# Performance work log

Measured on AMD Instinct MI355X. Metric: run time of the kernel, lower is better.

The kernel has to match this reference:

```python
import jax, jax.numpy as jnp
import numpy as np

L, B, E = 128, 16, 512
C_OUT = 64
KERNELS = [1, 3, 5, 7]
M = len(KERNELS) * C_OUT          # mlpdec_in = 256
OUT_SIZE = 256
SLOPE = 0.1


def setup_inputs() -> dict:
    key = jax.random.key(0)
    ks = jax.random.split(key, 32)
    s = 0.02
    d = {"x": jax.random.normal(ks[0], (L, B, E), dtype=jnp.float32)}
    # conv branches: weight (C_out, 1, k, E), bias (C_out,)
    for i, k in enumerate(KERNELS):
        d[f"cw{i}"] = jax.random.normal(ks[1 + 2 * i], (C_OUT, 1, k, E), dtype=jnp.float32) * s
        d[f"cb{i}"] = jnp.zeros((C_OUT,), dtype=jnp.float32)
    dims = [(C_OUT, 2 * M), (C_OUT, C_OUT), (C_OUT, C_OUT), (C_OUT, C_OUT)]
    for i, (o, inn) in enumerate(dims):
        d[f"mw{i}"] = jax.random.normal(ks[10 + 2 * i], (o, inn), dtype=jnp.float32) * s
        d[f"mb{i}"] = jnp.zeros((o,), dtype=jnp.float32)
    # mlp_layer: Linear(C->C), Linear(C->output_size)
    d["lw0"] = jax.random.normal(ks[20], (C_OUT, C_OUT), dtype=jnp.float32) * s
    d["lb0"] = jnp.zeros((C_OUT,), dtype=jnp.float32)
    d["lw1"] = jax.random.normal(ks[21], (OUT_SIZE, C_OUT), dtype=jnp.float32) * s
    d["lb1"] = jnp.zeros((OUT_SIZE,), dtype=jnp.float32)
    return d


def _lrelu(x):
    return jax.nn.leaky_relu(x, SLOPE)


def _conv_branch(xb, w, b):
    # xb: (B,1,L,E), w: (C,1,k,E) -> (B,C,L)
    k = w.shape[2]
    pad = (k - 1) // 2
    y = jax.lax.conv_general_dilated(
        xb, w, window_strides=(1, 1), padding=[(pad, pad), (0, 0)],
        dimension_numbers=("NCHW", "OIHW", "NCHW"))
    return _lrelu(y[..., 0] + b[None, :, None])


def reference(x, cw0, cb0, cw1, cb1, cw2, cb2, cw3, cb3,
              mw0, mb0, mw1, mb1, mw2, mb2, mw3, mb3,
              lw0, lb0, lw1, lb1):
    # x: (L,B,E) -> (B,1,L,E)
    xb = jnp.transpose(x, (1, 0, 2))[:, None, :, :]
    feats = jnp.concatenate([
        _conv_branch(xb, cw0, cb0), _conv_branch(xb, cw1, cb1),
        _conv_branch(xb, cw2, cb2), _conv_branch(xb, cw3, cb3)], axis=1)  # (B, 4C, L)
    f = jnp.transpose(feats, (2, 0, 1))  # (L, B, M)
    # pairwise: pair[i, j] = [f[j], f[i]]  -> (L, L, B, 2M)
    a = jnp.broadcast_to(f[None, :, :, :], (L, L, B, M))
    bpart = jnp.broadcast_to(f[:, None, :, :], (L, L, B, M))
    h = jnp.concatenate([a, bpart], axis=-1)
    for w, bb in ((mw0, mb0), (mw1, mb1), (mw2, mb2), (mw3, mb3)):
        h = _lrelu(h @ w.T + bb)
    h = h.sum(axis=0)  # (L, B, C)
    h = _lrelu(h @ lw0.T + lb0)
    return _lrelu(h @ lw1.T + lb1)  # (L, B, OUT_SIZE)
```

## Files before the change

### kernel.cpp

```cpp
#include <hip/hip_runtime.h>
#include <hip/hip_bf16.h>

#define SLOPE 0.1f
typedef unsigned short u16;
typedef unsigned int u32;
typedef __attribute__((ext_vector_type(8))) short short8;
typedef __attribute__((ext_vector_type(4))) float floatx4;

__device__ __forceinline__ float lrelu(float x) { return x > 0.0f ? x : SLOPE * x; }

__device__ __forceinline__ void split_rn(float x, u16* h, u16* l) {
    union { __hip_bfloat16 b; u16 u; } c1, c2;
    c1.b = __float2bfloat16(x);
    float hf = __bfloat162float(c1.b);
    c2.b = __float2bfloat16(x - hf);
    *h = c1.u; *l = c2.u;
}

__device__ __forceinline__ void pack2x2(float v0, float v1, u32& h, u32& l) {
    u32 a0 = __float_as_uint(v0), a1 = __float_as_uint(v1);
    h = __builtin_amdgcn_perm(a1, a0, 0x07060302u);
    float r0 = v0 - __uint_as_float(a0 & 0xFFFF0000u);
    float r1 = v1 - __uint_as_float(a1 & 0xFFFF0000u);
    l = __builtin_amdgcn_perm(__float_as_uint(r1), __float_as_uint(r0), 0x07060302u);
}

__device__ __forceinline__ short8 load_frag(const u16* p) {
    union { uint4 q; short8 s; } cv;
    cv.q = *(const uint4*)p;
    return cv.s;
}

__device__ __forceinline__ floatx4 mfma16(short8 a, short8 b, floatx4 c) {
    return __builtin_amdgcn_mfma_f32_16x16x32_bf16(a, b, c, 0, 0, 0);
}

__global__ __launch_bounds__(256) void p0_prep(
    const float* __restrict__ x,
    const float* __restrict__ cw0, const float* __restrict__ cw1,
    const float* __restrict__ cw2, const float* __restrict__ cw3,
    const float* __restrict__ mw0, const float* __restrict__ mw1,
    const float* __restrict__ mw2, const float* __restrict__ mw3,
    const float* __restrict__ lw0, const float* __restrict__ lw1,
    u16* __restrict__ xfh, u16* __restrict__ xfl,
    u16* __restrict__ wcfh, u16* __restrict__ wcfl,
    u16* __restrict__ b2fh, u16* __restrict__ b2fl,
    u16* __restrict__ w3fh, u16* __restrict__ w3fl,
    float* __restrict__ lw0t, float* __restrict__ lw1t)
{
    int idx = (blockIdx.x * 256 + threadIdx.x) * 4;
    if (idx < 1048576) {
        const int j = idx & 7, lane = (idx >> 3) & 63;
        const int kc = (idx >> 9) & 15, rt = idx >> 13;
        const int l15 = lane & 15, quad = lane >> 4;
        const float4 s = *(const float4*)(x + (rt * 16 + l15) * 512 + kc * 32 + quad * 8 + j);
        u16 h[4], l[4];
        split_rn(s.x, &h[0], &l[0]); split_rn(s.y, &h[1], &l[1]);
        split_rn(s.z, &h[2], &l[2]); split_rn(s.w, &h[3], &l[3]);
        *(ushort4*)(xfh + idx) = make_ushort4(h[0], h[1], h[2], h[3]);
        *(ushort4*)(xfl + idx) = make_ushort4(l[0], l[1], l[2], l[3]);
        return;
    }
    idx -= 1048576;
    if (idx < 524288) {
        const int j = idx & 7, lane = (idx >> 3) & 63;
        const int kc = (idx >> 9) & 15, nt = (idx >> 13) & 3, slot = idx >> 15;
        int branch, base;
        if (slot == 0)      { branch = 0; base = 0; }
        else if (slot < 4)  { branch = 1; base = 1; }
        else if (slot < 9)  { branch = 2; base = 4; }
        else                { branch = 3; base = 9; }
        const int dk = slot - base, ksz = 2 * branch + 1;
        const float* cw = branch == 0 ? cw0 : branch == 1 ? cw1 : branch == 2 ? cw2 : cw3;
        const int c = nt * 16 + (lane & 15);
        const int e = kc * 32 + (lane >> 4) * 8 + j;
        const float4 s = *(const float4*)(cw + (c * ksz + dk) * 512 + e);
        u16 h[4], l[4];
        split_rn(s.x, &h[0], &l[0]); split_rn(s.y, &h[1], &l[1]);
        split_rn(s.z, &h[2], &l[2]); split_rn(s.w, &h[3], &l[3]);
        *(ushort4*)(wcfh + idx) = make_ushort4(h[0], h[1], h[2], h[3]);
        *(ushort4*)(wcfl + idx) = make_ushort4(l[0], l[1], l[2], l[3]);
        return;
    }
    idx -= 524288;
    if (idx < 32768) {
        const int j = idx & 7, lane = (idx >> 3) & 63;
        const int kc = (idx >> 9) & 7, nt = (idx >> 12) & 3, nh = idx >> 14;
        const int n = nh * 64 + nt * 16 + (lane & 15);
        const int k = kc * 32 + (lane >> 4) * 8 + j;
        const float4 s = *(const float4*)(mw0 + (n & 63) * 512 + (n >> 6) * 256 + k);
        u16 h[4], l[4];
        split_rn(s.x, &h[0], &l[0]); split_rn(s.y, &h[1], &l[1]);
        split_rn(s.z, &h[2], &l[2]); split_rn(s.w, &h[3], &l[3]);
        *(ushort4*)(b2fh + idx) = make_ushort4(h[0], h[1], h[2], h[3]);
        *(ushort4*)(b2fl + idx) = make_ushort4(l[0], l[1], l[2], l[3]);
        return;
    }
    idx -= 32768;
    if (idx < 12288) {
        const int j = idx & 7, lane = (idx >> 3) & 63;
        const int kc = (idx >> 9) & 1, mt = (idx >> 10) & 3, layer = idx >> 12;
        const float* mw = layer == 0 ? mw1 : layer == 1 ? mw2 : mw3;
        const int ch = mt * 16 + (lane & 15);
        const int k = kc * 32 + (lane >> 4) * 8 + j;
        const float4 s = *(const float4*)(mw + ch * 64 + k);
        u16 h[4], l[4];
        split_rn(s.x, &h[0], &l[0]); split_rn(s.y, &h[1], &l[1]);
        split_rn(s.z, &h[2], &l[2]); split_rn(s.w, &h[3], &l[3]);
        *(ushort4*)(w3fh + idx) = make_ushort4(h[0], h[1], h[2], h[3]);
        *(ushort4*)(w3fl + idx) = make_ushort4(l[0], l[1], l[2], l[3]);
        return;
    }
    idx -= 12288;
    if (idx < 4096) {
        const int k = idx >> 6, n = idx & 63;
        float4 o;
        o.x = lw0[(n + 0) * 64 + k]; o.y = lw0[(n + 1) * 64 + k];
        o.z = lw0[(n + 2) * 64 + k]; o.w = lw0[(n + 3) * 64 + k];
        *(float4*)(lw0t + idx) = o;
        return;
    }
    idx -= 4096;
    if (idx < 16384) {
        const int k = idx >> 8, n = idx & 255;
        float4 o;
        o.x = lw1[(n + 0) * 64 + k]; o.y = lw1[(n + 1) * 64 + k];
        o.z = lw1[(n + 2) * 64 + k]; o.w = lw1[(n + 3) * 64 + k];
        *(float4*)(lw1t + idx) = o;
        return;
    }
}

__global__ __launch_bounds__(512) void k1f_conv(
    const u16* __restrict__ xfh, const u16* __restrict__ xfl,
    const u16* __restrict__ wcfh, const u16* __restrict__ wcfl,
    float* __restrict__ Fp)
{
    __shared__ float P[8][16][72];

    const int t = threadIdx.x, lane = t & 63, w = t >> 6;
    const int rtp = blockIdx.x;
    const int slot = blockIdx.y;
    int br, base;
    if (slot == 0)      { br = 0; base = 0; }
    else if (slot < 4)  { br = 1; base = 1; }
    else if (slot < 9)  { br = 2; base = 4; }
    else                { br = 3; base = 9; }
    const int dk = slot - base;
    const int l15 = lane & 15, quad = lane >> 4;

    floatx4 acc[2][4];
    #pragma unroll
    for (int r = 0; r < 2; ++r)
        #pragma unroll
        for (int j = 0; j < 4; ++j) acc[r][j] = (floatx4)0.0f;

    #pragma unroll
    for (int kk = 0; kk < 2; ++kk) {
        const int kc = w * 2 + kk;
        short8 bh[4], bl[4];
        #pragma unroll
        for (int nt = 0; nt < 4; ++nt) {
            const int boff = (((slot * 4 + nt) * 16 + kc) * 64 + lane) * 8;
            bh[nt] = load_frag(wcfh + boff);
            bl[nt] = load_frag(wcfl + boff);
        }
        #pragma unroll
        for (int r = 0; r < 2; ++r) {
            const int rts = rtp + r * 64 + dk - br;
            if (rts < 0 || rts >= 128) continue;
            const int aoff = ((rts * 16 + kc) * 64 + lane) * 8;
            const short8 ah = load_frag(xfh + aoff);
            const short8 al = load_frag(xfl + aoff);
            #pragma unroll
            for (int nt = 0; nt < 4; ++nt) {
                acc[r][nt] = mfma16(ah, bh[nt], acc[r][nt]);
                acc[r][nt] = mfma16(ah, bl[nt], acc[r][nt]);
                acc[r][nt] = mfma16(al, bh[nt], acc[r][nt]);
            }
        }
    }

    #pragma unroll
    for (int r = 0; r < 2; ++r) {
        #pragma unroll
        for (int nt = 0; nt < 4; ++nt)
            #pragma unroll
            for (int rr = 0; rr < 4; ++rr)
                P[w][quad * 4 + rr][nt * 16 + l15] = acc[r][nt][rr];
        __syncthreads();
        if (t < 256) {
            const int row = t >> 4, c4 = (t & 15) * 4;
            float4 o;
            #pragma unroll
            for (int i = 0; i < 4; ++i) {
                float val = P[0][row][c4 + i];
                #pragma unroll
                for (int ww = 1; ww < 8; ++ww) val += P[ww][row][c4 + i];
                (&o.x)[i] = val;
            }
            const int rowg = (rtp + r * 64) * 16 + row;
            *(float4*)(Fp + (slot * 2048 + rowg) * 64 + c4) = o;
        }
        __syncthreads();
    }
}

__global__ __launch_bounds__(256) void k2_uv(
    const float* __restrict__ Fp,
    const u16* __restrict__ b2fh, const u16* __restrict__ b2fl,
    const float* __restrict__ cb0, const float* __restrict__ cb1,
    const float* __restrict__ cb2, const float* __restrict__ cb3,
    const float* __restrict__ mb0,
    float* __restrict__ u, float* __restrict__ v_t)
{
    __shared__ float P[4][16][72];

    const int t = threadIdx.x, lane = t & 63, w = t >> 6;
    const int rt = blockIdx.x;
    const int nh = blockIdx.y;
    const int l15 = lane & 15, quad = lane >> 4;

    floatx4 acc[4];
    #pragma unroll
    for (int j = 0; j < 4; ++j) acc[j] = (floatx4)0.0f;

    #pragma unroll
    for (int kk = 0; kk < 2; ++kk) {
        const int kc = w * 2 + kk;
        const int br = kc >> 1;
        const int base = br * br, ksz = 2 * br + 1;
        const int cc0 = (kc & 1) * 32 + quad * 8;
        const int row = rt * 16 + l15;

        float s[8];
        #pragma unroll
        for (int j = 0; j < 8; ++j) s[j] = 0.0f;
        for (int d = 0; d < ksz; ++d) {
            const float* p = Fp + ((base + d) * 2048 + row) * 64 + cc0;
            const float4 q0 = *(const float4*)p;
            const float4 q1 = *(const float4*)(p + 4);
            s[0] += q0.x; s[1] += q0.y; s[2] += q0.z; s[3] += q0.w;
            s[4] += q1.x; s[5] += q1.y; s[6] += q1.z; s[7] += q1.w;
        }
        const float* cb = br == 0 ? cb0 : br == 1 ? cb1 : br == 2 ? cb2 : cb3;
        union { u16 us[8]; short8 v; } AH, AL;
        #pragma unroll
        for (int j = 0; j < 8; ++j) {
            const float val = lrelu(s[j] + cb[cc0 + j]);
            split_rn(val, &AH.us[j], &AL.us[j]);
        }
        const short8 ah = AH.v, al = AL.v;

        #pragma unroll
        for (int nt = 0; nt < 4; ++nt) {
            const int boff = (((nh * 4 + nt) * 8 + kc) * 64 + lane) * 8;
            const short8 bh = load_frag(b2fh + boff);
            const short8 bl = load_frag(b2fl + boff);
            acc[nt] = mfma16(ah, bh, acc[nt]);
            acc[nt] = mfma16(ah, bl, acc[nt]);
            acc[nt] = mfma16(al, bh, acc[nt]);
        }
    }

    #pragma unroll
    for (int nt = 0; nt < 4; ++nt)
        #pragma unroll
        for (int r = 0; r < 4; ++r)
            P[w][quad * 4 + r][nt * 16 + l15] = acc[nt][r];
    __syncthreads();

    const int row = t >> 4, c4 = (t & 15) * 4;
    const int rglob = rt * 16 + row;
    float4 oo;
    #pragma unroll
    for (int i = 0; i < 4; ++i)
        (&oo.x)[i] = P[0][row][c4 + i] + P[1][row][c4 + i]
                   + P[2][row][c4 + i] + P[3][row][c4 + i];
    if (nh == 0) {
        oo.x += mb0[c4 + 0]; oo.y += mb0[c4 + 1];
        oo.z += mb0[c4 + 2]; oo.w += mb0[c4 + 3];
        *(float4*)(u + rglob * 64 + c4) = oo;
    } else {
        const int i = rglob >> 4, b = rglob & 15;
        *(float4*)(v_t + (b * 128 + i) * 64 + c4) = oo;
    }
}

__global__ __launch_bounds__(256, 4) void k3_pair(
    const float* __restrict__ u, const float* __restrict__ v_t,
    const u16* __restrict__ w3fh, const u16* __restrict__ w3fl,
    const float* __restrict__ mb1, const float* __restrict__ mb2,
    const float* __restrict__ mb3,
    const float* __restrict__ lw0t, const float* __restrict__ lb0,
    const float* __restrict__ lw1t, const float* __restrict__ lb1,
    float* __restrict__ out)
{
    __shared__ __align__(16) u16 Hh[128][72];
    __shared__ __align__(16) u16 Hl[128][72];
    __shared__ float Sp[4][64];
    __shared__ float Ss[64];
    __shared__ float T1[64];

    const int t = threadIdx.x, lane = t & 63, w = t >> 6;
    const int jb = blockIdx.x, b = jb & 15;
    const int l15 = lane & 15, quad = lane >> 4;
    const int i0 = w * 32;
    const int c4 = l15 * 4;

    const float4 uu = *(const float4*)(u + jb * 64 + c4);

    const float* vb = v_t + (b * 128 + i0) * 64;
    #pragma unroll
    for (int n = 0; n < 8; ++n) {
        const int idx = n * 64 + lane;
        const int il = idx >> 4;
        const float4 vv = *(const float4*)(vb + idx * 4);
        const float a0 = lrelu(vv.x + uu.x), a1 = lrelu(vv.y + uu.y);
        const float a2 = lrelu(vv.z + uu.z), a3 = lrelu(vv.w + uu.w);
        u32 h01, l01, h23, l23;
        pack2x2(a0, a1, h01, l01);
        pack2x2(a2, a3, h23, l23);
        *(uint2*)&Hh[i0 + il][c4] = make_uint2(h01, h23);
        *(uint2*)&Hl[i0 + il][c4] = make_uint2(l01, l23);
    }

    const float* mbp[3] = {mb1, mb2, mb3};
    for (int layer = 0; layer < 3; ++layer) {
        floatx4 acc[4][2];
        #pragma unroll
        for (int i = 0; i < 4; ++i)
            #pragma unroll
            for (int j = 0; j < 2; ++j) acc[i][j] = (floatx4)0.0f;

        #pragma unroll
        for (int kc = 0; kc < 2; ++kc) {
            short8 ah[4], al[4];
            #pragma unroll
            for (int mt = 0; mt < 4; ++mt) {
                const int aoff = (((layer * 4 + mt) * 2 + kc) * 64 + lane) * 8;
                ah[mt] = load_frag(w3fh + aoff);
                al[mt] = load_frag(w3fl + aoff);
            }
            const int k0 = kc * 32 + quad * 8;
            #pragma unroll
            for (int nt = 0; nt < 2; ++nt) {
                const short8 bh = load_frag(&Hh[i0 + nt * 16 + l15][k0]);
                const short8 bl = load_frag(&Hl[i0 + nt * 16 + l15][k0]);
                #pragma unroll
                for (int mt = 0; mt < 4; ++mt) {
                    acc[mt][nt] = mfma16(ah[mt], bh, acc[mt][nt]);
                    acc[mt][nt] = mfma16(ah[mt], bl, acc[mt][nt]);
                    acc[mt][nt] = mfma16(al[mt], bh, acc[mt][nt]);
                }
            }
        }

        if (layer < 2) {
            #pragma unroll
            for (int mt = 0; mt < 4; ++mt) {
                float bias[4];
                #pragma unroll
                for (int r = 0; r < 4; ++r) bias[r] = mbp[layer][mt * 16 + quad * 4 + r];
                #pragma unroll
                for (int nt = 0; nt < 2; ++nt) {
                    const int i = i0 + nt * 16 + l15;
                    const float v0 = lrelu(acc[mt][nt][0] + bias[0]);
                    const float v1 = lrelu(acc[mt][nt][1] + bias[1]);
                    const float v2 = lrelu(acc[mt][nt][2] + bias[2]);
                    const float v3 = lrelu(acc[mt][nt][3] + bias[3]);
                    u32 h01, l01, h23, l23;
                    pack2x2(v0, v1, h01, l01);
                    pack2x2(v2, v3, h23, l23);
                    *(uint2*)&Hh[i][mt * 16 + quad * 4] = make_uint2(h01, h23);
                    *(uint2*)&Hl[i][mt * 16 + quad * 4] = make_uint2(l01, l23);
                }
            }
        } else {
            #pragma unroll
            for (int mt = 0; mt < 4; ++mt) {
                float bias[4];
                #pragma unroll
                for (int r = 0; r < 4; ++r) bias[r] = mbp[2][mt * 16 + quad * 4 + r];
                float4 sv;
                #pragma unroll
                for (int r = 0; r < 4; ++r) {
                    float val = lrelu(acc[mt][0][r] + bias[r])
                              + lrelu(acc[mt][1][r] + bias[r]);
                    val += __shfl_xor(val, 1, 16);
                    val += __shfl_xor(val, 2, 16);
                    val += __shfl_xor(val, 4, 16);
                    val += __shfl_xor(val, 8, 16);
                    (&sv.x)[r] = val;
                }
                if (l15 == 0)
                    *(float4*)(&Sp[w][mt * 16 + quad * 4]) = sv;
            }
        }
    }

    __syncthreads();
    if (t < 64) Ss[t] = Sp[0][t] + Sp[1][t] + Sp[2][t] + Sp[3][t];
    __syncthreads();
    if (t < 64) {
        float a = lb0[t];
        #pragma unroll 8
        for (int k = 0; k < 64; ++k) a += Ss[k] * lw0t[k * 64 + t];
        T1[t] = lrelu(a);
    }
    __syncthreads();
    {
        float a = lb1[t];
        #pragma unroll 8
        for (int k = 0; k < 64; ++k) a += T1[k] * lw1t[k * 256 + t];
        out[jb * 256 + t] = lrelu(a);
    }
}

extern "C" void kernel_launch(void* const* d_in, const int* in_sizes, int n_in,
                              void* d_out, int out_size, void* d_ws, size_t ws_size,
                              hipStream_t stream)
{
    const float* x   = (const float*)d_in[0];
    const float* cw0 = (const float*)d_in[1];
    const float* cb0 = (const float*)d_in[2];
    const float* cw1 = (const float*)d_in[3];
    const float* cb1 = (const float*)d_in[4];
    const float* cw2 = (const float*)d_in[5];
    const float* cb2 = (const float*)d_in[6];
    const float* cw3 = (const float*)d_in[7];
    const float* cb3 = (const float*)d_in[8];
    const float* mw0 = (const float*)d_in[9];
    const float* mb0 = (const float*)d_in[10];
    const float* mw1 = (const float*)d_in[11];
    const float* mb1 = (const float*)d_in[12];
    const float* mw2 = (const float*)d_in[13];
    const float* mb2 = (const float*)d_in[14];
    const float* mw3 = (const float*)d_in[15];
    const float* mb3 = (const float*)d_in[16];
    const float* lw0 = (const float*)d_in[17];
    const float* lb0 = (const float*)d_in[18];
    const float* lw1 = (const float*)d_in[19];
    const float* lb1 = (const float*)d_in[20];
    float* out = (float*)d_out;

    char* base = (char*)d_ws;
    u16* xfh   = (u16*)(base + 0);
    u16* xfl   = (u16*)(base + 2097152);
    u16* wcfh  = (u16*)(base + 4194304);
    u16* wcfl  = (u16*)(base + 5242880);
    u16* b2fh  = (u16*)(base + 6291456);
    u16* b2fl  = (u16*)(base + 6356992);
    u16* w3fh  = (u16*)(base + 6422528);
    u16* w3fl  = (u16*)(base + 6447104);
    float* lw0t  = (float*)(base + 6471680);
    float* lw1t  = (float*)(base + 6488064);
    float* Fp  = (float*)(base + 6553600);
    float* u   = (float*)(base + 14942208);
    float* v_t = (float*)(base + 15466496);

    hipLaunchKernelGGL(p0_prep, dim3(1600), dim3(256), 0, stream,
                       x, cw0, cw1, cw2, cw3, mw0, mw1, mw2, mw3, lw0, lw1,
                       xfh, xfl, wcfh, wcfl, b2fh, b2fl, w3fh, w3fl, lw0t, lw1t);
    hipLaunchKernelGGL(k1f_conv, dim3(64, 16), dim3(512), 0, stream,
                       xfh, xfl, wcfh, wcfl, Fp);
    hipLaunchKernelGGL(k2_uv, dim3(128, 2), dim3(256), 0, stream,
                       Fp, b2fh, b2fl, cb0, cb1, cb2, cb3, mb0, u, v_t);
    hipLaunchKernelGGL(k3_pair, dim3(2048), dim3(256), 0, stream,
                       u, v_t, w3fh, w3fl, mb1, mb2, mb3, lw0t, lb0, lw1t, lb1, out);
}
```

Before: 151.9 us.

## Fuse input/weight bf16 splitting into conv kernel and widen uv grid

The prep kernel no longer pre-splits x and conv weights into bf16 hi/lo fragment buffers. The conv kernel now loads fp32 directly and splits in registers, and small weight prep runs in an extra grid row of the conv kernel. This removes one launch and a round trip of about 6 MB through global memory. The uv kernel is split into 1024 blocks that each compute one 16-column tile, to expose more parallelism. The trade-off is redundant split work across conv blocks and uncoalesced fp32 loads in place of prepacked fragment loads.

```diff
diff --git a/kernel.cpp b/kernel.cpp
--- a/kernel.cpp
+++ b/kernel.cpp
@@ -17,6 +17,17 @@
     *h = c1.u; *l = c2.u;
 }
 
+__device__ __forceinline__ void split8(const float* __restrict__ p, short8& h8, short8& l8) {
+    union { u16 us[8]; short8 v; } H, L;
+    const float4 a = *(const float4*)p;
+    const float4 b = *(const float4*)(p + 4);
+    split_rn(a.x, &H.us[0], &L.us[0]); split_rn(a.y, &H.us[1], &L.us[1]);
+    split_rn(a.z, &H.us[2], &L.us[2]); split_rn(a.w, &H.us[3], &L.us[3]);
+    split_rn(b.x, &H.us[4], &L.us[4]); split_rn(b.y, &H.us[5], &L.us[5]);
+    split_rn(b.z, &H.us[6], &L.us[6]); split_rn(b.w, &H.us[7], &L.us[7]);
+    h8 = H.v; l8 = L.v;
+}
+
 __device__ __forceinline__ void pack2x2(float v0, float v1, u32& h, u32& l) {
     u32 a0 = __float_as_uint(v0), a1 = __float_as_uint(v1);
     h = __builtin_amdgcn_perm(a1, a0, 0x07060302u);
@@ -35,54 +46,14 @@
     return __builtin_amdgcn_mfma_f32_16x16x32_bf16(a, b, c, 0, 0, 0);
 }
 
-__global__ __launch_bounds__(256) void p0_prep(
-    const float* __restrict__ x,
-    const float* __restrict__ cw0, const float* __restrict__ cw1,
-    const float* __restrict__ cw2, const float* __restrict__ cw3,
+__device__ __forceinline__ void prep_tail(int idx,
     const float* __restrict__ mw0, const float* __restrict__ mw1,
     const float* __restrict__ mw2, const float* __restrict__ mw3,
     const float* __restrict__ lw0, const float* __restrict__ lw1,
-    u16* __restrict__ xfh, u16* __restrict__ xfl,
-    u16* __restrict__ wcfh, u16* __restrict__ wcfl,
     u16* __restrict__ b2fh, u16* __restrict__ b2fl,
     u16* __restrict__ w3fh, u16* __restrict__ w3fl,
     float* __restrict__ lw0t, float* __restrict__ lw1t)
 {
-    int idx = (blockIdx.x * 256 + threadIdx.x) * 4;
-    if (idx < 1048576) {
-        const int j = idx & 7, lane = (idx >> 3) & 63;
-        const int kc = (idx >> 9) & 15, rt = idx >> 13;
-        const int l15 = lane & 15, quad = lane >> 4;
-        const float4 s = *(const float4*)(x + (rt * 16 + l15) * 512 + kc * 32 + quad * 8 + j);
-        u16 h[4], l[4];
-        split_rn(s.x, &h[0], &l[0]); split_rn(s.y, &h[1], &l[1]);
-        split_rn(s.z, &h[2], &l[2]); split_rn(s.w, &h[3], &l[3]);
-        *(ushort4*)(xfh + idx) = make_ushort4(h[0], h[1], h[2], h[3]);
-        *(ushort4*)(xfl + idx) = make_ushort4(l[0], l[1], l[2], l[3]);
-        return;
-    }
-    idx -= 1048576;
-    if (idx < 524288) {
-        const int j = idx & 7, lane = (idx >> 3) & 63;
-        const int kc = (idx >> 9) & 15, nt = (idx >> 13) & 3, slot = idx >> 15;
-        int branch, base;
-        if (slot == 0)      { branch = 0; base = 0; }
-        else if (slot < 4)  { branch = 1; base = 1; }
-        else if (slot < 9)  { branch = 2; base = 4; }
-        else                { branch = 3; base = 9; }
-        const int dk = slot - base, ksz = 2 * branch + 1;
-        const float* cw = branch == 0 ? cw0 : branch == 1 ? cw1 : branch == 2 ? cw2 : cw3;
-        const int c = nt * 16 + (lane & 15);
-        const int e = kc * 32 + (lane >> 4) * 8 + j;
-        const float4 s = *(const float4*)(cw + (c * ksz + dk) * 512 + e);
-        u16 h[4], l[4];
-        split_rn(s.x, &h[0], &l[0]); split_rn(s.y, &h[1], &l[1]);
-        split_rn(s.z, &h[2], &l[2]); split_rn(s.w, &h[3], &l[3]);
-        *(ushort4*)(wcfh + idx) = make_ushort4(h[0], h[1], h[2], h[3]);
-        *(ushort4*)(wcfl + idx) = make_ushort4(l[0], l[1], l[2], l[3]);
-        return;
-    }
-    idx -= 524288;
     if (idx < 32768) {
         const int j = idx & 7, lane = (idx >> 3) & 63;
         const int kc = (idx >> 9) & 7, nt = (idx >> 12) & 3, nh = idx >> 14;
@@ -131,23 +102,40 @@
     }
 }
 
-__global__ __launch_bounds__(512) void k1f_conv(
-    const u16* __restrict__ xfh, const u16* __restrict__ xfl,
-    const u16* __restrict__ wcfh, const u16* __restrict__ wcfl,
+__global__ __launch_bounds__(512) void kA_conv(
+    const float* __restrict__ x,
+    const float* __restrict__ cw0, const float* __restrict__ cw1,
+    const float* __restrict__ cw2, const float* __restrict__ cw3,
+    const float* __restrict__ mw0, const float* __restrict__ mw1,
+    const float* __restrict__ mw2, const float* __restrict__ mw3,
+    const float* __restrict__ lw0, const float* __restrict__ lw1,
+    u16* __restrict__ b2fh, u16* __restrict__ b2fl,
+    u16* __restrict__ w3fh, u16* __restrict__ w3fl,
+    float* __restrict__ lw0t, float* __restrict__ lw1t,
     float* __restrict__ Fp)
 {
     __shared__ float P[8][16][72];
 
     const int t = threadIdx.x, lane = t & 63, w = t >> 6;
+    const int slot = blockIdx.y;
+
+    if (slot == 16) {
+        const int gid = blockIdx.x * 512 + t;
+        if (gid < 16384)
+            prep_tail(gid * 4, mw0, mw1, mw2, mw3, lw0, lw1,
+                      b2fh, b2fl, w3fh, w3fl, lw0t, lw1t);
+        return;
+    }
+
     const int rtp = blockIdx.x;
-    const int slot = blockIdx.y;
     int br, base;
     if (slot == 0)      { br = 0; base = 0; }
     else if (slot < 4)  { br = 1; base = 1; }
     else if (slot < 9)  { br = 2; base = 4; }
     else                { br = 3; base = 9; }
-    const int dk = slot - base;
+    const int dk = slot - base, ksz = 2 * br + 1;
     const int l15 = lane & 15, quad = lane >> 4;
+    const float* cw = br == 0 ? cw0 : br == 1 ? cw1 : br == 2 ? cw2 : cw3;
 
     floatx4 acc[2][4];
     #pragma unroll
@@ -158,20 +146,19 @@
     #pragma unroll
     for (int kk = 0; kk < 2; ++kk) {
         const int kc = w * 2 + kk;
+        const int e0 = kc * 32 + quad * 8;
         short8 bh[4], bl[4];
         #pragma unroll
         for (int nt = 0; nt < 4; ++nt) {
-            const int boff = (((slot * 4 + nt) * 16 + kc) * 64 + lane) * 8;
-            bh[nt] = load_frag(wcfh + boff);
-            bl[nt] = load_frag(wcfl + boff);
+            const int c = nt * 16 + l15;
+            split8(cw + (c * ksz + dk) * 512 + e0, bh[nt], bl[nt]);
         }
         #pragma unroll
         for (int r = 0; r < 2; ++r) {
             const int rts = rtp + r * 64 + dk - br;
             if (rts < 0 || rts >= 128) continue;
-            const int aoff = ((rts * 16 + kc) * 64 + lane) * 8;
-            const short8 ah = load_frag(xfh + aoff);
-            const short8 al = load_frag(xfl + aoff);
+            short8 ah, al;
+            split8(x + (rts * 16 + l15) * 512 + e0, ah, al);
             #pragma unroll
             for (int nt = 0; nt < 4; ++nt) {
                 acc[r][nt] = mfma16(ah, bh[nt], acc[r][nt]);
@@ -206,7 +193,7 @@
     }
 }
 
-__global__ __launch_bounds__(256) void k2_uv(
+__global__ __launch_bounds__(256) void kB_uv(
     const float* __restrict__ Fp,
     const u16* __restrict__ b2fh, const u16* __restrict__ b2fl,
     const float* __restrict__ cb0, const float* __restrict__ cb1,
@@ -214,36 +201,36 @@
     const float* __restrict__ mb0,
     float* __restrict__ u, float* __restrict__ v_t)
 {
-    __shared__ float P[4][16][72];
+    __shared__ float P[4][16][17];
 
     const int t = threadIdx.x, lane = t & 63, w = t >> 6;
-    const int rt = blockIdx.x;
-    const int nh = blockIdx.y;
+    const int bid = blockIdx.x;
+    const int rt = bid >> 3;
+    const int nh = (bid >> 2) & 1;
+    const int nt = bid & 3;
     const int l15 = lane & 15, quad = lane >> 4;
 
-    floatx4 acc[4];
-    #pragma unroll
-    for (int j = 0; j < 4; ++j) acc[j] = (floatx4)0.0f;
+    floatx4 acc = (floatx4)0.0f;
 
     #pragma unroll
     for (int kk = 0; kk < 2; ++kk) {
         const int kc = w * 2 + kk;
-        const int br = kc >> 1;
-        const int base = br * br, ksz = 2 * br + 1;
+        const int br2 = kc >> 1;
+        const int base2 = br2 * br2, ksz2 = 2 * br2 + 1;
         const int cc0 = (kc & 1) * 32 + quad * 8;
         const int row = rt * 16 + l15;
 
         float s[8];
         #pragma unroll
         for (int j = 0; j < 8; ++j) s[j] = 0.0f;
-        for (int d = 0; d < ksz; ++d) {
-            const float* p = Fp + ((base + d) * 2048 + row) * 64 + cc0;
-            const float4 q0 = *(const float4*)p;
-            const float4 q1 = *(const float4*)(p + 4);
+        for (int d = 0; d < ksz2; ++d) {
+            const float* pp = Fp + ((base2 + d) * 2048 + row) * 64 + cc0;
+            const float4 q0 = *(const float4*)pp;
+            const float4 q1 = *(const float4*)(pp + 4);
             s[0] += q0.x; s[1] += q0.y; s[2] += q0.z; s[3] += q0.w;
             s[4] += q1.x; s[5] += q1.y; s[6] += q1.z; s[7] += q1.w;
         }
-        const float* cb = br == 0 ? cb0 : br == 1 ? cb1 : br == 2 ? cb2 : cb3;
+        const float* cb = br2 == 0 ? cb0 : br2 == 1 ? cb1 : br2 == 2 ? cb2 : cb3;
         union { u16 us[8]; short8 v; } AH, AL;
         #pragma unroll
         for (int j = 0; j < 8; ++j) {
@@ -252,42 +239,34 @@
         }
         const short8 ah = AH.v, al = AL.v;
 
-        #pragma unroll
-        for (int nt = 0; nt < 4; ++nt) {
-            const int boff = (((nh * 4 + nt) * 8 + kc) * 64 + lane) * 8;
-            const short8 bh = load_frag(b2fh + boff);
-            const short8 bl = load_frag(b2fl + boff);
-            acc[nt] = mfma16(ah, bh, acc[nt]);
-            acc[nt] = mfma16(ah, bl, acc[nt]);
-            acc[nt] = mfma16(al, bh, acc[nt]);
-        }
-    }
-
-    #pragma unroll
-    for (int nt = 0; nt < 4; ++nt)
-        #pragma unroll
-        for (int r = 0; r < 4; ++r)
-            P[w][quad * 4 + r][nt * 16 + l15] = acc[nt][r];
+        const int boff = (((nh * 4 + nt) * 8 + kc) * 64 + lane) * 8;
+        const short8 bh = load_frag(b2fh + boff);
+        const short8 bl = load_frag(b2fl + boff);
+        acc = mfma16(ah, bh, acc);
+        acc = mfma16(ah, bl, acc);
+        acc = mfma16(al, bh, acc);
+    }
+
+    #pragma unroll
+    for (int rr = 0; rr < 4; ++rr)
+        P[w][quad * 4 + rr][l15] = acc[rr];
     __syncthreads();
 
-    const int row = t >> 4, c4 = (t & 15) * 4;
-    const int rglob = rt * 16 + row;
-    float4 oo;
-    #pragma unroll
-    for (int i = 0; i < 4; ++i)
-        (&oo.x)[i] = P[0][row][c4 + i] + P[1][row][c4 + i]
-                   + P[2][row][c4 + i] + P[3][row][c4 + i];
-    if (nh == 0) {
-        oo.x += mb0[c4 + 0]; oo.y += mb0[c4 + 1];
-        oo.z += mb0[c4 + 2]; oo.w += mb0[c4 + 3];
-        *(float4*)(u + rglob * 64 + c4) = oo;
-    } else {
-        const int i = rglob >> 4, b = rglob & 15;
-        *(float4*)(v_t + (b * 128 + i) * 64 + c4) = oo;
-    }
-}
-
-__global__ __launch_bounds__(256, 4) void k3_pair(
+    {
+        const int row = t >> 4, c = t & 15;
+        const float val = P[0][row][c] + P[1][row][c] + P[2][row][c] + P[3][row][c];
+        const int rglob = rt * 16 + row;
+        const int ch = nt * 16 + c;
+        if (nh == 0) {
+            u[rglob * 64 + ch] = val + mb0[ch];
+        } else {
+            const int i = rglob >> 4, b = rglob & 15;
+            v_t[(b * 128 + i) * 64 + ch] = val;
+        }
+    }
+}
+
+__global__ __launch_bounds__(256, 4) void kC_pair(
     const float* __restrict__ u, const float* __restrict__ v_t,
     const u16* __restrict__ w3fh, const u16* __restrict__ w3fl,
     const float* __restrict__ mb1, const float* __restrict__ mb2,
@@ -445,27 +424,21 @@
     float* out = (float*)d_out;
 
     char* base = (char*)d_ws;
-    u16* xfh   = (u16*)(base + 0);
-    u16* xfl   = (u16*)(base + 2097152);
-    u16* wcfh  = (u16*)(base + 4194304);
-    u16* wcfl  = (u16*)(base + 5242880);
-    u16* b2fh  = (u16*)(base + 6291456);
-    u16* b2fl  = (u16*)(base + 6356992);
-    u16* w3fh  = (u16*)(base + 6422528);
-    u16* w3fl  = (u16*)(base + 6447104);
-    float* lw0t  = (float*)(base + 6471680);
-    float* lw1t  = (float*)(base + 6488064);
-    float* Fp  = (float*)(base + 6553600);
-    float* u   = (float*)(base + 14942208);
-    float* v_t = (float*)(base + 15466496);
-
-    hipLaunchKernelGGL(p0_prep, dim3(1600), dim3(256), 0, stream,
+    u16* b2fh   = (u16*)(base + 0);
+    u16* b2fl   = (u16*)(base + 65536);
+    u16* w3fh   = (u16*)(base + 131072);
+    u16* w3fl   = (u16*)(base + 155648);
+    float* lw0t = (float*)(base + 180224);
+    float* lw1t = (float*)(base + 196608);
+    float* Fp   = (float*)(base + 262144);
+    float* u    = (float*)(base + 8650752);
+    float* v_t  = (float*)(base + 9175040);
+
+    hipLaunchKernelGGL(kA_conv, dim3(64, 17), dim3(512), 0, stream,
                        x, cw0, cw1, cw2, cw3, mw0, mw1, mw2, mw3, lw0, lw1,
-                       xfh, xfl, wcfh, wcfl, b2fh, b2fl, w3fh, w3fl, lw0t, lw1t);
-    hipLaunchKernelGGL(k1f_conv, dim3(64, 16), dim3(512), 0, stream,
-                       xfh, xfl, wcfh, wcfl, Fp);
-    hipLaunchKernelGGL(k2_uv, dim3(128, 2), dim3(256), 0, stream,
+                       b2fh, b2fl, w3fh, w3fl, lw0t, lw1t, Fp);
+    hipLaunchKernelGGL(kB_uv, dim3(1024), dim3(256), 0, stream,
                        Fp, b2fh, b2fl, cb0, cb1, cb2, cb3, mb0, u, v_t);
-    hipLaunchKernelGGL(k3_pair, dim3(2048), dim3(256), 0, stream,
+    hipLaunchKernelGGL(kC_pair, dim3(2048), dim3(256), 0, stream,
                        u, v_t, w3fh, w3fl, mb1, mb2, mb3, lw0t, lb0, lw1t, lb1, out);
 }
```

New measurement: 165.7 us. 1.09x slower.
